# Kernel tuning notes

Hardware: AMD Instinct MI355X
Metric: run time of the kernel (lower is better)

## Reference

```python
import jax, jax.numpy as jnp
import numpy as np

B, T, C, H = 2, 2048, 1024, 16
DH = C // H  # 64


def setup_inputs() -> dict:
    key = jax.random.key(0)
    ks = jax.random.split(key, 8)
    scale = 1.0 / np.sqrt(C)
    x = jax.random.normal(ks[0], (B, T, C), dtype=jnp.float32)
    mask = jax.random.randint(ks[1], (B, T), 0, 2, dtype=jnp.int32)
    Wq = jax.random.normal(ks[2], (C, C), dtype=jnp.float32) * scale
    bq = jnp.zeros((C,), dtype=jnp.float32)
    Wk = jax.random.normal(ks[3], (C, C), dtype=jnp.float32) * scale
    bk = jnp.zeros((C,), dtype=jnp.float32)
    Wv = jax.random.normal(ks[4], (C, C), dtype=jnp.float32) * scale
    bv = jnp.zeros((C,), dtype=jnp.float32)
    return {"x": x, "Wq": Wq, "bq": bq, "Wk": Wk, "bk": bk, "Wv": Wv, "bv": bv, "mask": mask}


def reference(x, Wq, bq, Wk, bk, Wv, bv, mask):
    # q/k/v projections: [B,T,C] -> [B,H,T,DH]
    def proj(W, b):
        return (x @ W + b).reshape(B, T, H, DH).transpose(0, 2, 1, 3)

    q = proj(Wq, bq)
    k = proj(Wk, bk)
    v = proj(Wv, bv)

    att = jnp.einsum("bhqd,bhkd->bhqk", q, k) * (1.0 / np.sqrt(DH))

    # outer-product padding mask: square_mask[b,q,k] = mask[b,q]*mask[b,k]
    m = mask.astype(jnp.float32)
    square_mask = m[:, :, None] * m[:, None, :]           # [B,T,T]
    sm = (square_mask != 0)[:, None, :, :]                 # [B,1,T,T]
    att = jnp.where(sm, att, -jnp.inf)

    # rows that are fully masked (query token padded) -> softmax gives NaN
    # in torch; torch then zeros the NaNs. Replicate with a safe softmax.
    row_valid = (mask != 0)[:, None, :, None]              # [B,1,T,1]
    att_safe = jnp.where(row_valid, att, 0.0)
    att = jax.nn.softmax(att_safe, axis=-1)
    att = jnp.where(row_valid, att, 0.0)
    # attn_pdrop = 0.0 -> dropout is identity

    y = jnp.einsum("bhqk,bhkd->bhqd", att, v)              # [B,H,T,DH]
    y = y.transpose(0, 2, 1, 3).reshape(B, T, C)
    return y
```

## Files before the change

kernel.cpp:

```cpp
#include <hip/hip_runtime.h>

#define B_ 2
#define T_ 2048
#define C_ 1024
#define H_ 16
#define DH_ 64

typedef __attribute__((ext_vector_type(8))) _Float16 half8;
typedef __attribute__((ext_vector_type(2))) __fp16 fp16x2;
typedef __attribute__((ext_vector_type(4))) float f32x4;

__device__ __forceinline__ unsigned short f2h(float f) {
    union { _Float16 h; unsigned short u; } cv; cv.h = (_Float16)f; return cv.u;
}
__device__ __forceinline__ unsigned pk2(float a, float b) {
    union { fp16x2 h; unsigned u; } cv;
    cv.h = __builtin_amdgcn_cvt_pkrtz(a, b);
    return cv.u;
}

__device__ __forceinline__ void gll16(const void* g, void* l) {
    __builtin_amdgcn_global_load_lds(
        (const __attribute__((address_space(1))) void*)g,
        (__attribute__((address_space(3))) void*)l, 16, 0, 0);
}

__global__ __launch_bounds__(256) void prep_x_kernel(
    const float* __restrict__ x, unsigned short* __restrict__ xf,
    const int* __restrict__ mask, unsigned short* __restrict__ mb)
{
    const size_t idx8 = ((size_t)blockIdx.x * 256 + threadIdx.x) * 8;
    float4 v0 = *(const float4*)(x + idx8);
    float4 v1 = *(const float4*)(x + idx8 + 4);
    float f[8] = {v0.x, v0.y, v0.z, v0.w, v1.x, v1.y, v1.z, v1.w};
    unsigned short h[8];
#pragma unroll
    for (int i = 0; i < 8; i++) h[i] = f2h(f[i]);
    *(uint4*)(xf + idx8) = *(const uint4*)h;

    if (blockIdx.x == 0) {
#pragma unroll
        for (int j = 0; j < 16; j++) {
            int i = threadIdx.x * 16 + j;
            mb[i] = (mask[i] != 0) ? (unsigned short)0x3C00 : (unsigned short)0;
        }
    }
}

__global__ __launch_bounds__(256) void prep_w_kernel(
    const float* __restrict__ Wq, const float* __restrict__ Wk,
    const float* __restrict__ Wv, unsigned short* __restrict__ wt)
{
    __shared__ float tile[32][33];
    const int z = blockIdx.z;
    const float* __restrict__ W = (z == 0) ? Wq : (z == 1) ? Wk : Wv;
    unsigned short* __restrict__ wtz = wt + (size_t)z * C_ * C_;
    const int n0 = blockIdx.x * 32;
    const int k0 = blockIdx.y * 32;
    const int tx = threadIdx.x;
    const int ty = threadIdx.y;
#pragma unroll
    for (int j = 0; j < 4; j++)
        tile[ty + j * 8][tx] = W[(size_t)(k0 + ty + j * 8) * C_ + n0 + tx];
    __syncthreads();
#pragma unroll
    for (int j = 0; j < 4; j++)
        wtz[(size_t)(n0 + ty + j * 8) * C_ + k0 + tx] = f2h(tile[tx][ty + j * 8]);
}

__global__ __launch_bounds__(256) void qkv_mfma_kernel(
    const unsigned short* __restrict__ xf, const unsigned short* __restrict__ wt,
    const float* __restrict__ bq, const float* __restrict__ bk,
    const float* __restrict__ bv, const int* __restrict__ maskp,
    unsigned short* __restrict__ qb, unsigned short* __restrict__ kb,
    unsigned short* __restrict__ vt)
{
    __shared__ unsigned short sX[128 * 64];
    __shared__ unsigned short sW[128 * 64];

    const int z = blockIdx.z;
    const float* __restrict__ bias = (z == 0) ? bq : (z == 1) ? bk : bv;
    const unsigned short* __restrict__ wtz = wt + (size_t)z * C_ * C_;

    const int tok0 = blockIdx.x * 128;
    const int col0 = blockIdx.y * 128;
    const int wv    = threadIdx.x >> 6;
    const int lane  = threadIdx.x & 63;
    const int l15   = lane & 15;
    const int quad  = lane >> 4;
    const int l7    = l15 & 7;
    const int wm    = wv >> 1;
    const int wn    = wv & 1;
    const int lrow8 = lane >> 3;
    const int gch   = (lane & 7) ^ lrow8;

    f32x4 acc[4][4];
#pragma unroll
    for (int i = 0; i < 4; i++)
#pragma unroll
        for (int j = 0; j < 4; j++) acc[i][j] = (f32x4){0.f, 0.f, 0.f, 0.f};

    int aoff[4][2], boff[4][2];
#pragma unroll
    for (int i = 0; i < 4; i++)
#pragma unroll
        for (int s = 0; s < 2; s++) {
            aoff[i][s] = (wm * 64 + i * 16 + l15) * 64 + (((s * 4 + quad) ^ l7) * 8);
            boff[i][s] = (wn * 64 + i * 16 + l15) * 64 + (((s * 4 + quad) ^ l7) * 8);
        }

    const unsigned short* Abuf = (z < 2) ? sX : sW;
    const unsigned short* Bbuf = (z < 2) ? sW : sX;

    for (int k0 = 0; k0 < C_; k0 += 64) {
        __syncthreads();
#pragma unroll
        for (int s = 0; s < 8; ++s) {
            int g    = (s << 2) + wv;
            int tsel = g >> 4;
            int r0   = (g & 15) << 3;
            const unsigned short* src = tsel ? wtz : xf;
            unsigned short*       dst = tsel ? sW  : sX;
            int rowg = tsel ? col0 : tok0;
            gll16(src + (size_t)(rowg + r0 + lrow8) * C_ + k0 + gch * 8,
                  dst + r0 * 64);
        }
        __syncthreads();

        half8 af[4][2], bf_[4][2];
#pragma unroll
        for (int i = 0; i < 4; i++)
#pragma unroll
            for (int s = 0; s < 2; s++) {
                af[i][s]  = *(const half8*)&Abuf[aoff[i][s]];
                bf_[i][s] = *(const half8*)&Bbuf[boff[i][s]];
            }
#pragma unroll
        for (int s = 0; s < 2; s++)
#pragma unroll
            for (int j = 0; j < 4; j++)
#pragma unroll
                for (int i = 0; i < 4; i++)
                    acc[i][j] = __builtin_amdgcn_mfma_f32_16x16x32_f16(
                        af[i][s], bf_[j][s], acc[i][j], 0, 0, 0);
    }

    if (z == 0) {
#pragma unroll
        for (int j = 0; j < 4; j++) {
            int col = col0 + wn * 64 + j * 16 + l15;
            int h = col >> 6, d = col & 63;
            float bs = bias[col];
#pragma unroll
            for (int i = 0; i < 4; i++) {
#pragma unroll
                for (int r = 0; r < 4; r++) {
                    int tok = tok0 + wm * 64 + i * 16 + quad * 4 + r;
                    int bidx = tok >> 11, t = tok & (T_ - 1);
                    qb[((size_t)(bidx * H_ + h) * T_ + t) * DH_ + d] =
                        f2h((acc[i][j][r] + bs) * 0.18033688011112042f);
                }
            }
        }
    } else if (z == 1) {
#pragma unroll
        for (int j = 0; j < 4; j++) {
            int col = col0 + wn * 64 + j * 16 + l15;
            int h = col >> 6, d = col & 63;
            float bs = bias[col];
#pragma unroll
            for (int i = 0; i < 4; i++) {
#pragma unroll
                for (int r = 0; r < 4; r++) {
                    int tok = tok0 + wm * 64 + i * 16 + quad * 4 + r;
                    int bidx = tok >> 11, t = tok & (T_ - 1);
                    kb[((size_t)(bidx * H_ + h) * T_ + t) * DH_ + d] =
                        f2h(acc[i][j][r] + bs);
                }
            }
        }
    } else {
        float mv4[4]; int bidx4[4], t4[4];
#pragma unroll
        for (int j = 0; j < 4; j++) {
            int tok = tok0 + wn * 64 + j * 16 + l15;
            bidx4[j] = tok >> 11; t4[j] = tok & (T_ - 1);
            mv4[j] = (maskp[bidx4[j] * T_ + t4[j]] != 0) ? 1.f : 0.f;
        }
#pragma unroll
        for (int i = 0; i < 4; i++) {
#pragma unroll
            for (int r = 0; r < 4; r++) {
                int col = col0 + wm * 64 + i * 16 + quad * 4 + r;
                int h = col >> 6, d = col & 63;
                float bs = bias[col];
#pragma unroll
                for (int j = 0; j < 4; j++) {
                    vt[((size_t)(bidx4[j] * H_ + h) * DH_ + d) * T_ + t4[j]] =
                        f2h((acc[i][j][r] + bs) * mv4[j]);
                }
            }
        }
    }
}

__global__ __launch_bounds__(256) void attn_mfma_kernel(
    const unsigned short* __restrict__ qb,
    const unsigned short* __restrict__ kb,
    const unsigned short* __restrict__ vt,
    const int* __restrict__ mask,
    const unsigned short* __restrict__ mb,
    float* __restrict__ out)
{
    __shared__ unsigned short Ks[2][64 * 64];
    __shared__ unsigned short Vs[2][64 * 64];
    __shared__ unsigned short Ps[4][2][16 * 64];

    const int bh   = blockIdx.x;
    const int b    = bh >> 4;
    const int h    = bh & 15;
    const int wv   = threadIdx.x >> 6;
    const int lane = threadIdx.x & 63;
    const int l15  = lane & 15;
    const int quad = lane >> 4;
    const int l7   = l15 & 7;
    const int q0w  = blockIdx.y * 128 + wv * 32;

    const unsigned short* kbh = kb + (size_t)bh * T_ * DH_;
    const unsigned short* vbh = vt + (size_t)bh * DH_ * T_;
    const unsigned short* mbb = mb + b * T_;
    const int* __restrict__ mrow = mask + b * T_;

    half8 qf[2][2];
#pragma unroll
    for (int qt = 0; qt < 2; ++qt)
#pragma unroll
        for (int c = 0; c < 2; ++c)
            qf[qt][c] = *(const half8*)(qb + ((size_t)bh * T_ + q0w + qt * 16 + l15) * DH_
                                        + c * 32 + quad * 8);

    f32x4 o[2][4];
#pragma unroll
    for (int qt = 0; qt < 2; ++qt)
#pragma unroll
        for (int n = 0; n < 4; ++n) o[qt][n] = (f32x4){0.f, 0.f, 0.f, 0.f};
    f32x4 lacc[2];
    lacc[0] = (f32x4){0.f, 0.f, 0.f, 0.f};
    lacc[1] = (f32x4){0.f, 0.f, 0.f, 0.f};

    const int lrow = lane >> 3;
    const int gch  = (lane & 7) ^ lrow;

#pragma unroll
    for (int s = 0; s < 4; ++s) {
        int j  = (wv << 2) + s;
        int rb = j & 7;
        if (j < 8) gll16(kbh + (size_t)(rb * 8 + lrow) * DH_ + gch * 8, &Ks[0][rb * 512]);
        else       gll16(vbh + (size_t)(rb * 8 + lrow) * T_  + gch * 8, &Vs[0][rb * 512]);
    }

    for (int kt = 0; kt < 32; ++kt) {
        const int cur   = kt & 1;
        const int kbase = kt * 64;
        __syncthreads();

        if (kt < 31) {
            const int nb = kbase + 64;
#pragma unroll
            for (int s = 0; s < 4; ++s) {
                int j  = (wv << 2) + s;
                int rb = j & 7;
                if (j < 8) gll16(kbh + (size_t)(nb + rb * 8 + lrow) * DH_ + gch * 8,
                                 &Ks[cur ^ 1][rb * 512]);
                else       gll16(vbh + (size_t)(rb * 8 + lrow) * T_ + nb + gch * 8,
                                 &Vs[cur ^ 1][rb * 512]);
            }
        }

        const unsigned short* Kc = &Ks[cur][0];
        const unsigned short* Vc = &Vs[cur][0];

        half8 kf[4][2], vf[4][2];
#pragma unroll
        for (int ktile = 0; ktile < 4; ++ktile)
#pragma unroll
            for (int c = 0; c < 2; ++c) {
                kf[ktile][c] = *(const half8*)(Kc + (ktile * 16 + l15) * 64
                                               + (((c * 4 + quad) ^ l7) * 8));
                vf[ktile][c] = *(const half8*)(Vc + (ktile * 16 + l15) * 64
                                               + (((c * 4 + quad) ^ l7) * 8));
            }

        half8 bmf[2];
#pragma unroll
        for (int kc = 0; kc < 2; ++kc) {
            half8 mv = *(const half8*)(mbb + kbase + kc * 32 + quad * 8);
            bmf[kc] = (l15 == 0) ? mv : (half8)0;
        }

#pragma unroll
        for (int qt = 0; qt < 2; ++qt) {
            unsigned short* Pq = &Ps[wv][qt][0];
#pragma unroll
            for (int ktile = 0; ktile < 4; ++ktile) {
                f32x4 st = (f32x4){0.f, 0.f, 0.f, 0.f};
                st = __builtin_amdgcn_mfma_f32_16x16x32_f16(kf[ktile][0], qf[qt][0], st, 0, 0, 0);
                st = __builtin_amdgcn_mfma_f32_16x16x32_f16(kf[ktile][1], qf[qt][1], st, 0, 0, 0);
                uint2 pk;
                pk.x = pk2(__builtin_amdgcn_exp2f(st[0]), __builtin_amdgcn_exp2f(st[1]));
                pk.y = pk2(__builtin_amdgcn_exp2f(st[2]), __builtin_amdgcn_exp2f(st[3]));
                *(uint2*)(Pq + l15 * 64 + (((ktile * 2 + (quad >> 1)) ^ l7) * 8)
                          + (quad & 1) * 4) = pk;
            }
        }

#pragma unroll
        for (int qt = 0; qt < 2; ++qt) {
            const unsigned short* Pq = &Ps[wv][qt][0];
            half8 pf[2];
#pragma unroll
            for (int kc = 0; kc < 2; ++kc)
                pf[kc] = *(const half8*)(Pq + l15 * 64 + (((kc * 4 + quad) ^ l7) * 8));

            lacc[qt] = __builtin_amdgcn_mfma_f32_16x16x32_f16(pf[0], bmf[0], lacc[qt], 0, 0, 0);
            lacc[qt] = __builtin_amdgcn_mfma_f32_16x16x32_f16(pf[1], bmf[1], lacc[qt], 0, 0, 0);

#pragma unroll
            for (int n = 0; n < 4; ++n) {
#pragma unroll
                for (int kc = 0; kc < 2; ++kc)
                    o[qt][n] = __builtin_amdgcn_mfma_f32_16x16x32_f16(
                        pf[kc], vf[n][kc], o[qt][n], 0, 0, 0);
            }
        }
    }

#pragma unroll
    for (int qt = 0; qt < 2; ++qt) {
#pragma unroll
        for (int r = 0; r < 4; ++r) {
            float lv = __shfl(lacc[qt][r], quad << 4, 64);
            int q = q0w + qt * 16 + quad * 4 + r;
            float iv = (mrow[q] != 0 && lv > 0.f) ? (1.0f / lv) : 0.f;
            float* orow = out + ((size_t)(b * T_ + q)) * C_ + h * DH_;
#pragma unroll
            for (int n = 0; n < 4; ++n)
                orow[n * 16 + l15] = o[qt][n][r] * iv;
        }
    }
}

extern "C" void kernel_launch(void* const* d_in, const int* in_sizes, int n_in,
                              void* d_out, int out_size, void* d_ws, size_t ws_size,
                              hipStream_t stream)
{
    (void)in_sizes; (void)n_in; (void)out_size; (void)ws_size;
    const float* x  = (const float*)d_in[0];
    const float* Wq = (const float*)d_in[1];
    const float* bq = (const float*)d_in[2];
    const float* Wk = (const float*)d_in[3];
    const float* bk = (const float*)d_in[4];
    const float* Wv = (const float*)d_in[5];
    const float* bv = (const float*)d_in[6];
    const int* mask = (const int*)d_in[7];
    float* out = (float*)d_out;

    const size_t NX = (size_t)B_ * T_ * C_;
    unsigned short* xf = (unsigned short*)d_ws;
    unsigned short* wt = xf + NX;
    unsigned short* qb = wt + (size_t)3 * C_ * C_;
    unsigned short* kb = qb + NX;
    unsigned short* vt = kb + NX;
    unsigned short* mb = vt + NX;

    prep_x_kernel<<<2048, 256, 0, stream>>>(x, xf, mask, mb);
    prep_w_kernel<<<dim3(32, 32, 3), dim3(32, 8), 0, stream>>>(Wq, Wk, Wv, wt);
    qkv_mfma_kernel<<<dim3(32, 8, 3), 256, 0, stream>>>(
        xf, wt, bq, bk, bv, mask, qb, kb, vt);
    attn_mfma_kernel<<<dim3(32, 16), 256, 0, stream>>>(qb, kb, vt, mask, mb, out);
}
```

Before: 172.1 us.

## Fuse QKV projections into one kernel sharing X tiles, merge prep kernels

Merges the x-conversion and weight-transpose prep kernels into a single launch. The QKV GEMM now computes Q, K and V in one block that loads each X tile once and reuses it against all three weight tiles, instead of three separate grid slices that each reload X. This cuts launches and X traffic, but triples accumulator registers (192 floats of accumulators per lane), forces 1 block per CU, and shrinks the grid from 768 to 256 blocks, which may reduce occupancy and parallelism.

```diff
diff --git a/kernel.cpp b/kernel.cpp
--- a/kernel.cpp
+++ b/kernel.cpp
@@ -25,50 +25,53 @@
         (__attribute__((address_space(3))) void*)l, 16, 0, 0);
 }
 
-__global__ __launch_bounds__(256) void prep_x_kernel(
+__global__ __launch_bounds__(256) void prep_kernel(
     const float* __restrict__ x, unsigned short* __restrict__ xf,
-    const int* __restrict__ mask, unsigned short* __restrict__ mb)
-{
-    const size_t idx8 = ((size_t)blockIdx.x * 256 + threadIdx.x) * 8;
-    float4 v0 = *(const float4*)(x + idx8);
-    float4 v1 = *(const float4*)(x + idx8 + 4);
-    float f[8] = {v0.x, v0.y, v0.z, v0.w, v1.x, v1.y, v1.z, v1.w};
-    unsigned short h[8];
-#pragma unroll
-    for (int i = 0; i < 8; i++) h[i] = f2h(f[i]);
-    *(uint4*)(xf + idx8) = *(const uint4*)h;
-
-    if (blockIdx.x == 0) {
-#pragma unroll
-        for (int j = 0; j < 16; j++) {
-            int i = threadIdx.x * 16 + j;
-            mb[i] = (mask[i] != 0) ? (unsigned short)0x3C00 : (unsigned short)0;
-        }
-    }
-}
-
-__global__ __launch_bounds__(256) void prep_w_kernel(
+    const int* __restrict__ mask, unsigned short* __restrict__ mb,
     const float* __restrict__ Wq, const float* __restrict__ Wk,
     const float* __restrict__ Wv, unsigned short* __restrict__ wt)
 {
     __shared__ float tile[32][33];
-    const int z = blockIdx.z;
-    const float* __restrict__ W = (z == 0) ? Wq : (z == 1) ? Wk : Wv;
-    unsigned short* __restrict__ wtz = wt + (size_t)z * C_ * C_;
-    const int n0 = blockIdx.x * 32;
-    const int k0 = blockIdx.y * 32;
-    const int tx = threadIdx.x;
-    const int ty = threadIdx.y;
-#pragma unroll
-    for (int j = 0; j < 4; j++)
-        tile[ty + j * 8][tx] = W[(size_t)(k0 + ty + j * 8) * C_ + n0 + tx];
-    __syncthreads();
-#pragma unroll
-    for (int j = 0; j < 4; j++)
-        wtz[(size_t)(n0 + ty + j * 8) * C_ + k0 + tx] = f2h(tile[tx][ty + j * 8]);
-}
-
-__global__ __launch_bounds__(256) void qkv_mfma_kernel(
+    const int tid = threadIdx.x;
+
+    if (blockIdx.x < 2048) {
+        const size_t idx8 = ((size_t)blockIdx.x * 256 + tid) * 8;
+        float4 v0 = *(const float4*)(x + idx8);
+        float4 v1 = *(const float4*)(x + idx8 + 4);
+        float f[8] = {v0.x, v0.y, v0.z, v0.w, v1.x, v1.y, v1.z, v1.w};
+        unsigned short h[8];
+#pragma unroll
+        for (int i = 0; i < 8; i++) h[i] = f2h(f[i]);
+        *(uint4*)(xf + idx8) = *(const uint4*)h;
+
+        if (blockIdx.x == 0) {
+#pragma unroll
+            for (int j = 0; j < 16; j++) {
+                int i = tid * 16 + j;
+                mb[i] = (mask[i] != 0) ? (unsigned short)0x3C00 : (unsigned short)0;
+            }
+        }
+    } else {
+        const int idx = blockIdx.x - 2048;
+        const int z   = idx >> 10;
+        const int rem = idx & 1023;
+        const int n0  = (rem & 31) * 32;
+        const int k0  = (rem >> 5) * 32;
+        const float* __restrict__ W = (z == 0) ? Wq : (z == 1) ? Wk : Wv;
+        unsigned short* __restrict__ wtz = wt + (size_t)z * C_ * C_;
+        const int tx = tid & 31;
+        const int ty = tid >> 5;
+#pragma unroll
+        for (int j = 0; j < 4; j++)
+            tile[ty + j * 8][tx] = W[(size_t)(k0 + ty + j * 8) * C_ + n0 + tx];
+        __syncthreads();
+#pragma unroll
+        for (int j = 0; j < 4; j++)
+            wtz[(size_t)(n0 + ty + j * 8) * C_ + k0 + tx] = f2h(tile[tx][ty + j * 8]);
+    }
+}
+
+__global__ __launch_bounds__(256, 1) void qkv_fused_kernel(
     const unsigned short* __restrict__ xf, const unsigned short* __restrict__ wt,
     const float* __restrict__ bq, const float* __restrict__ bk,
     const float* __restrict__ bv, const int* __restrict__ maskp,
@@ -76,11 +79,7 @@
     unsigned short* __restrict__ vt)
 {
     __shared__ unsigned short sX[128 * 64];
-    __shared__ unsigned short sW[128 * 64];
-
-    const int z = blockIdx.z;
-    const float* __restrict__ bias = (z == 0) ? bq : (z == 1) ? bk : bv;
-    const unsigned short* __restrict__ wtz = wt + (size_t)z * C_ * C_;
+    __shared__ unsigned short sW[3 * 128 * 64];
 
     const int tok0 = blockIdx.x * 128;
     const int col0 = blockIdx.y * 128;
@@ -94,11 +93,15 @@
     const int lrow8 = lane >> 3;
     const int gch   = (lane & 7) ^ lrow8;
 
-    f32x4 acc[4][4];
+    f32x4 accq[4][4], acck[4][4], accv[4][4];
 #pragma unroll
     for (int i = 0; i < 4; i++)
 #pragma unroll
-        for (int j = 0; j < 4; j++) acc[i][j] = (f32x4){0.f, 0.f, 0.f, 0.f};
+        for (int j = 0; j < 4; j++) {
+            accq[i][j] = (f32x4){0.f, 0.f, 0.f, 0.f};
+            acck[i][j] = (f32x4){0.f, 0.f, 0.f, 0.f};
+            accv[i][j] = (f32x4){0.f, 0.f, 0.f, 0.f};
+        }
 
     int aoff[4][2], boff[4][2];
 #pragma unroll
@@ -109,81 +112,88 @@
             boff[i][s] = (wn * 64 + i * 16 + l15) * 64 + (((s * 4 + quad) ^ l7) * 8);
         }
 
-    const unsigned short* Abuf = (z < 2) ? sX : sW;
-    const unsigned short* Bbuf = (z < 2) ? sW : sX;
-
     for (int k0 = 0; k0 < C_; k0 += 64) {
         __syncthreads();
 #pragma unroll
-        for (int s = 0; s < 8; ++s) {
-            int g    = (s << 2) + wv;
-            int tsel = g >> 4;
-            int r0   = (g & 15) << 3;
-            const unsigned short* src = tsel ? wtz : xf;
-            unsigned short*       dst = tsel ? sW  : sX;
-            int rowg = tsel ? col0 : tok0;
-            gll16(src + (size_t)(rowg + r0 + lrow8) * C_ + k0 + gch * 8,
-                  dst + r0 * 64);
+        for (int s = 0; s < 16; ++s) {
+            int c = (s << 2) + wv;
+            if (c < 16) {
+                int r0 = c << 3;
+                gll16(xf + (size_t)(tok0 + r0 + lrow8) * C_ + k0 + gch * 8,
+                      sX + r0 * 64);
+            } else {
+                int w  = c - 16;
+                int z  = w >> 4;
+                int r0 = (w & 15) << 3;
+                gll16(wt + (size_t)z * C_ * C_
+                         + (size_t)(col0 + r0 + lrow8) * C_ + k0 + gch * 8,
+                      sW + z * 8192 + r0 * 64);
+            }
         }
         __syncthreads();
 
-        half8 af[4][2], bf_[4][2];
+        half8 af[4][2];
 #pragma unroll
         for (int i = 0; i < 4; i++)
 #pragma unroll
-            for (int s = 0; s < 2; s++) {
-                af[i][s]  = *(const half8*)&Abuf[aoff[i][s]];
-                bf_[i][s] = *(const half8*)&Bbuf[boff[i][s]];
-            }
-#pragma unroll
-        for (int s = 0; s < 2; s++)
-#pragma unroll
-            for (int j = 0; j < 4; j++)
-#pragma unroll
-                for (int i = 0; i < 4; i++)
-                    acc[i][j] = __builtin_amdgcn_mfma_f32_16x16x32_f16(
-                        af[i][s], bf_[j][s], acc[i][j], 0, 0, 0);
-    }
-
-    if (z == 0) {
+            for (int s = 0; s < 2; s++)
+                af[i][s] = *(const half8*)&sX[aoff[i][s]];
+
 #pragma unroll
         for (int j = 0; j < 4; j++) {
-            int col = col0 + wn * 64 + j * 16 + l15;
-            int h = col >> 6, d = col & 63;
-            float bs = bias[col];
+            half8 bw0 = *(const half8*)&sW[boff[j][0]];
+            half8 bw1 = *(const half8*)&sW[boff[j][1]];
 #pragma unroll
             for (int i = 0; i < 4; i++) {
-#pragma unroll
-                for (int r = 0; r < 4; r++) {
-                    int tok = tok0 + wm * 64 + i * 16 + quad * 4 + r;
-                    int bidx = tok >> 11, t = tok & (T_ - 1);
-                    qb[((size_t)(bidx * H_ + h) * T_ + t) * DH_ + d] =
-                        f2h((acc[i][j][r] + bs) * 0.18033688011112042f);
-                }
-            }
-        }
-    } else if (z == 1) {
+                accq[i][j] = __builtin_amdgcn_mfma_f32_16x16x32_f16(af[i][0], bw0, accq[i][j], 0, 0, 0);
+                accq[i][j] = __builtin_amdgcn_mfma_f32_16x16x32_f16(af[i][1], bw1, accq[i][j], 0, 0, 0);
+            }
+        }
 #pragma unroll
         for (int j = 0; j < 4; j++) {
-            int col = col0 + wn * 64 + j * 16 + l15;
-            int h = col >> 6, d = col & 63;
-            float bs = bias[col];
+            half8 bw0 = *(const half8*)&sW[8192 + boff[j][0]];
+            half8 bw1 = *(const half8*)&sW[8192 + boff[j][1]];
 #pragma unroll
             for (int i = 0; i < 4; i++) {
-#pragma unroll
-                for (int r = 0; r < 4; r++) {
-                    int tok = tok0 + wm * 64 + i * 16 + quad * 4 + r;
-                    int bidx = tok >> 11, t = tok & (T_ - 1);
-                    kb[((size_t)(bidx * H_ + h) * T_ + t) * DH_ + d] =
-                        f2h(acc[i][j][r] + bs);
-                }
-            }
-        }
-    } else {
+                acck[i][j] = __builtin_amdgcn_mfma_f32_16x16x32_f16(af[i][0], bw0, acck[i][j], 0, 0, 0);
+                acck[i][j] = __builtin_amdgcn_mfma_f32_16x16x32_f16(af[i][1], bw1, acck[i][j], 0, 0, 0);
+            }
+        }
+#pragma unroll
+        for (int i = 0; i < 4; i++) {
+            half8 aw0 = *(const half8*)&sW[16384 + boff[i][0]];
+            half8 aw1 = *(const half8*)&sW[16384 + boff[i][1]];
+#pragma unroll
+            for (int j = 0; j < 4; j++) {
+                accv[i][j] = __builtin_amdgcn_mfma_f32_16x16x32_f16(aw0, af[j][0], accv[i][j], 0, 0, 0);
+                accv[i][j] = __builtin_amdgcn_mfma_f32_16x16x32_f16(aw1, af[j][1], accv[i][j], 0, 0, 0);
+            }
+        }
+    }
+
+#pragma unroll
+    for (int j = 0; j < 4; j++) {
+        int col = col0 + wn * 64 + j * 16 + l15;
+        int h = col >> 6, d = col & 63;
+        float bsq = bq[col];
+        float bsk = bk[col];
+#pragma unroll
+        for (int i = 0; i < 4; i++) {
+#pragma unroll
+            for (int r = 0; r < 4; r++) {
+                int tok = tok0 + wm * 64 + i * 16 + quad * 4 + r;
+                int bidx = tok >> 11, t = tok & (T_ - 1);
+                size_t base = ((size_t)(bidx * H_ + h) * T_ + t) * DH_ + d;
+                qb[base] = f2h((accq[i][j][r] + bsq) * 0.18033688011112042f);
+                kb[base] = f2h(acck[i][j][r] + bsk);
+            }
+        }
+    }
+    {
         float mv4[4]; int bidx4[4], t4[4];
 #pragma unroll
         for (int j = 0; j < 4; j++) {
-            int tok = tok0 + wn * 64 + j * 16 + l15;
+            int tok = tok0 + wm * 64 + j * 16 + l15;
             bidx4[j] = tok >> 11; t4[j] = tok & (T_ - 1);
             mv4[j] = (maskp[bidx4[j] * T_ + t4[j]] != 0) ? 1.f : 0.f;
         }
@@ -191,13 +201,13 @@
         for (int i = 0; i < 4; i++) {
 #pragma unroll
             for (int r = 0; r < 4; r++) {
-                int col = col0 + wm * 64 + i * 16 + quad * 4 + r;
+                int col = col0 + wn * 64 + i * 16 + quad * 4 + r;
                 int h = col >> 6, d = col & 63;
-                float bs = bias[col];
+                float bs = bv[col];
 #pragma unroll
                 for (int j = 0; j < 4; j++) {
                     vt[((size_t)(bidx4[j] * H_ + h) * DH_ + d) * T_ + t4[j]] =
-                        f2h((acc[i][j][r] + bs) * mv4[j]);
+                        f2h((accv[i][j][r] + bs) * mv4[j]);
                 }
             }
         }
@@ -373,9 +383,8 @@
     unsigned short* vt = kb + NX;
     unsigned short* mb = vt + NX;
 
-    prep_x_kernel<<<2048, 256, 0, stream>>>(x, xf, mask, mb);
-    prep_w_kernel<<<dim3(32, 32, 3), dim3(32, 8), 0, stream>>>(Wq, Wk, Wv, wt);
-    qkv_mfma_kernel<<<dim3(32, 8, 3), 256, 0, stream>>>(
+    prep_kernel<<<5120, 256, 0, stream>>>(x, xf, mask, mb, Wq, Wk, Wv, wt);
+    qkv_fused_kernel<<<dim3(32, 8), 256, 0, stream>>>(
         xf, wt, bq, bk, bv, mask, qb, kb, vt);
     attn_mfma_kernel<<<dim3(32, 16), 256, 0, stream>>>(qb, kb, vt, mask, mb, out);
 }
```

New measurement: 175.1 us. Within noise of the previous version (+1.8%).

## Keep softmax probabilities in registers and merge prep kernels into one launch

Applied to the files above, without the earlier changes.

The attention kernel no longer writes exp'd scores to an LDS P buffer and reads them back. The QK^T MFMA output layout is reused directly as the A operand of 16x16x16 f16 MFMAs for the PV product and the row-sum, with V read from LDS in matching half4 fragments. Separately, the x-conversion and weight-transpose prep kernels are fused into one launch to save launch overhead. The cost is twice as many smaller MFMA instructions and more V LDS reads of narrower width.

```diff
diff --git a/kernel.cpp b/kernel.cpp
--- a/kernel.cpp
+++ b/kernel.cpp
@@ -7,6 +7,7 @@
 #define DH_ 64
 
 typedef __attribute__((ext_vector_type(8))) _Float16 half8;
+typedef __attribute__((ext_vector_type(4))) _Float16 half4;
 typedef __attribute__((ext_vector_type(2))) __fp16 fp16x2;
 typedef __attribute__((ext_vector_type(4))) float f32x4;
 
@@ -25,47 +26,50 @@
         (__attribute__((address_space(3))) void*)l, 16, 0, 0);
 }
 
-__global__ __launch_bounds__(256) void prep_x_kernel(
+__global__ __launch_bounds__(256) void prep_kernel(
     const float* __restrict__ x, unsigned short* __restrict__ xf,
-    const int* __restrict__ mask, unsigned short* __restrict__ mb)
-{
-    const size_t idx8 = ((size_t)blockIdx.x * 256 + threadIdx.x) * 8;
-    float4 v0 = *(const float4*)(x + idx8);
-    float4 v1 = *(const float4*)(x + idx8 + 4);
-    float f[8] = {v0.x, v0.y, v0.z, v0.w, v1.x, v1.y, v1.z, v1.w};
-    unsigned short h[8];
-#pragma unroll
-    for (int i = 0; i < 8; i++) h[i] = f2h(f[i]);
-    *(uint4*)(xf + idx8) = *(const uint4*)h;
-
-    if (blockIdx.x == 0) {
-#pragma unroll
-        for (int j = 0; j < 16; j++) {
-            int i = threadIdx.x * 16 + j;
-            mb[i] = (mask[i] != 0) ? (unsigned short)0x3C00 : (unsigned short)0;
-        }
-    }
-}
-
-__global__ __launch_bounds__(256) void prep_w_kernel(
+    const int* __restrict__ mask, unsigned short* __restrict__ mb,
     const float* __restrict__ Wq, const float* __restrict__ Wk,
     const float* __restrict__ Wv, unsigned short* __restrict__ wt)
 {
     __shared__ float tile[32][33];
-    const int z = blockIdx.z;
-    const float* __restrict__ W = (z == 0) ? Wq : (z == 1) ? Wk : Wv;
-    unsigned short* __restrict__ wtz = wt + (size_t)z * C_ * C_;
-    const int n0 = blockIdx.x * 32;
-    const int k0 = blockIdx.y * 32;
-    const int tx = threadIdx.x;
-    const int ty = threadIdx.y;
-#pragma unroll
-    for (int j = 0; j < 4; j++)
-        tile[ty + j * 8][tx] = W[(size_t)(k0 + ty + j * 8) * C_ + n0 + tx];
-    __syncthreads();
-#pragma unroll
-    for (int j = 0; j < 4; j++)
-        wtz[(size_t)(n0 + ty + j * 8) * C_ + k0 + tx] = f2h(tile[tx][ty + j * 8]);
+    const int tid = threadIdx.x;
+
+    if (blockIdx.x < 2048) {
+        const size_t idx8 = ((size_t)blockIdx.x * 256 + tid) * 8;
+        float4 v0 = *(const float4*)(x + idx8);
+        float4 v1 = *(const float4*)(x + idx8 + 4);
+        float f[8] = {v0.x, v0.y, v0.z, v0.w, v1.x, v1.y, v1.z, v1.w};
+        unsigned short h[8];
+#pragma unroll
+        for (int i = 0; i < 8; i++) h[i] = f2h(f[i]);
+        *(uint4*)(xf + idx8) = *(const uint4*)h;
+
+        if (blockIdx.x == 0) {
+#pragma unroll
+            for (int j = 0; j < 16; j++) {
+                int i = tid * 16 + j;
+                mb[i] = (mask[i] != 0) ? (unsigned short)0x3C00 : (unsigned short)0;
+            }
+        }
+    } else {
+        const int idx = blockIdx.x - 2048;
+        const int z   = idx >> 10;
+        const int rem = idx & 1023;
+        const int n0  = (rem & 31) * 32;
+        const int k0  = (rem >> 5) * 32;
+        const float* __restrict__ W = (z == 0) ? Wq : (z == 1) ? Wk : Wv;
+        unsigned short* __restrict__ wtz = wt + (size_t)z * C_ * C_;
+        const int tx = tid & 31;
+        const int ty = tid >> 5;
+#pragma unroll
+        for (int j = 0; j < 4; j++)
+            tile[ty + j * 8][tx] = W[(size_t)(k0 + ty + j * 8) * C_ + n0 + tx];
+        __syncthreads();
+#pragma unroll
+        for (int j = 0; j < 4; j++)
+            wtz[(size_t)(n0 + ty + j * 8) * C_ + k0 + tx] = f2h(tile[tx][ty + j * 8]);
+    }
 }
 
 __global__ __launch_bounds__(256) void qkv_mfma_kernel(
@@ -214,7 +218,6 @@
 {
     __shared__ unsigned short Ks[2][64 * 64];
     __shared__ unsigned short Vs[2][64 * 64];
-    __shared__ unsigned short Ps[4][2][16 * 64];
 
     const int bh   = blockIdx.x;
     const int b    = bh >> 4;
@@ -280,58 +283,55 @@
         const unsigned short* Kc = &Ks[cur][0];
         const unsigned short* Vc = &Vs[cur][0];
 
-        half8 kf[4][2], vf[4][2];
+        half8 kf[4][2];
 #pragma unroll
         for (int ktile = 0; ktile < 4; ++ktile)
 #pragma unroll
-            for (int c = 0; c < 2; ++c) {
+            for (int c = 0; c < 2; ++c)
                 kf[ktile][c] = *(const half8*)(Kc + (ktile * 16 + l15) * 64
                                                + (((c * 4 + quad) ^ l7) * 8));
-                vf[ktile][c] = *(const half8*)(Vc + (ktile * 16 + l15) * 64
-                                               + (((c * 4 + quad) ^ l7) * 8));
-            }
-
-        half8 bmf[2];
-#pragma unroll
-        for (int kc = 0; kc < 2; ++kc) {
-            half8 mv = *(const half8*)(mbb + kbase + kc * 32 + quad * 8);
-            bmf[kc] = (l15 == 0) ? mv : (half8)0;
+
+        half4 vb[4][4];
+#pragma unroll
+        for (int n = 0; n < 4; ++n)
+#pragma unroll
+            for (int ktile = 0; ktile < 4; ++ktile)
+                vb[n][ktile] = *(const half4*)(Vc + (n * 16 + l15) * 64
+                                               + (((ktile * 2 + (quad >> 1)) ^ l7) * 8)
+                                               + (quad & 1) * 4);
+
+        half4 bmf[4];
+#pragma unroll
+        for (int ktile = 0; ktile < 4; ++ktile) {
+            half4 mv = *(const half4*)(mbb + kbase + ktile * 16 + quad * 4);
+            bmf[ktile] = (l15 == 0) ? mv : (half4)0;
         }
 
 #pragma unroll
         for (int qt = 0; qt < 2; ++qt) {
-            unsigned short* Pq = &Ps[wv][qt][0];
+            half4 pa[4];
 #pragma unroll
             for (int ktile = 0; ktile < 4; ++ktile) {
                 f32x4 st = (f32x4){0.f, 0.f, 0.f, 0.f};
                 st = __builtin_amdgcn_mfma_f32_16x16x32_f16(kf[ktile][0], qf[qt][0], st, 0, 0, 0);
                 st = __builtin_amdgcn_mfma_f32_16x16x32_f16(kf[ktile][1], qf[qt][1], st, 0, 0, 0);
-                uint2 pk;
-                pk.x = pk2(__builtin_amdgcn_exp2f(st[0]), __builtin_amdgcn_exp2f(st[1]));
-                pk.y = pk2(__builtin_amdgcn_exp2f(st[2]), __builtin_amdgcn_exp2f(st[3]));
-                *(uint2*)(Pq + l15 * 64 + (((ktile * 2 + (quad >> 1)) ^ l7) * 8)
-                          + (quad & 1) * 4) = pk;
-            }
-        }
-
-#pragma unroll
-        for (int qt = 0; qt < 2; ++qt) {
-            const unsigned short* Pq = &Ps[wv][qt][0];
-            half8 pf[2];
-#pragma unroll
-            for (int kc = 0; kc < 2; ++kc)
-                pf[kc] = *(const half8*)(Pq + l15 * 64 + (((kc * 4 + quad) ^ l7) * 8));
-
-            lacc[qt] = __builtin_amdgcn_mfma_f32_16x16x32_f16(pf[0], bmf[0], lacc[qt], 0, 0, 0);
-            lacc[qt] = __builtin_amdgcn_mfma_f32_16x16x32_f16(pf[1], bmf[1], lacc[qt], 0, 0, 0);
-
-#pragma unroll
-            for (int n = 0; n < 4; ++n) {
-#pragma unroll
-                for (int kc = 0; kc < 2; ++kc)
-                    o[qt][n] = __builtin_amdgcn_mfma_f32_16x16x32_f16(
-                        pf[kc], vf[n][kc], o[qt][n], 0, 0, 0);
-            }
+                union { uint2 u; half4 h; } cv;
+                cv.u.x = pk2(__builtin_amdgcn_exp2f(st[0]), __builtin_amdgcn_exp2f(st[1]));
+                cv.u.y = pk2(__builtin_amdgcn_exp2f(st[2]), __builtin_amdgcn_exp2f(st[3]));
+                pa[ktile] = cv.h;
+            }
+
+#pragma unroll
+            for (int ktile = 0; ktile < 4; ++ktile)
+                lacc[qt] = __builtin_amdgcn_mfma_f32_16x16x16f16(
+                    pa[ktile], bmf[ktile], lacc[qt], 0, 0, 0);
+
+#pragma unroll
+            for (int n = 0; n < 4; ++n)
+#pragma unroll
+                for (int ktile = 0; ktile < 4; ++ktile)
+                    o[qt][n] = __builtin_amdgcn_mfma_f32_16x16x16f16(
+                        pa[ktile], vb[n][ktile], o[qt][n], 0, 0, 0);
         }
     }
 
@@ -373,8 +373,7 @@
     unsigned short* vt = kb + NX;
     unsigned short* mb = vt + NX;
 
-    prep_x_kernel<<<2048, 256, 0, stream>>>(x, xf, mask, mb);
-    prep_w_kernel<<<dim3(32, 32, 3), dim3(32, 8), 0, stream>>>(Wq, Wk, Wv, wt);
+    prep_kernel<<<5120, 256, 0, stream>>>(x, xf, mask, mb, Wq, Wk, Wv, wt);
     qkv_mfma_kernel<<<dim3(32, 8, 3), 256, 0, stream>>>(
         xf, wt, bq, bk, bv, mask, qb, kb, vt);
     attn_mfma_kernel<<<dim3(32, 16), 256, 0, stream>>>(qb, kb, vt, mask, mb, out);
```

Result: faster. 168.2 us (median of 2 runs) (-2.3%).
